# Kernel tuning notes

Hardware: AMD Instinct MI355X
Metric: run time of the kernel (lower is better)

The kernel has to match this reference:

```python
import jax, jax.numpy as jnp
import numpy as np

H, DH, M = 8, 64, 3          # heads, dim_head, num memory tokens
DIM = 512                    # model dim
INNER = H * DH               # 512
SCALE = DH ** -0.5
SQRT_DH = float(np.sqrt(DH))
SQRT_M = float(np.sqrt(M))


def setup_inputs() -> dict:
    key = jax.random.key(0)
    ks = jax.random.split(key, 7)
    b, n = 2, 2048
    x = jax.random.normal(ks[0], (b, n, DIM), dtype=jnp.float32)
    # Linear weights stored as (in, out); y = x @ W
    wq = jax.random.normal(ks[1], (DIM, INNER), dtype=jnp.float32) * (DIM ** -0.5)
    wkv = jax.random.normal(ks[2], (DIM, 2 * INNER), dtype=jnp.float32) * (DIM ** -0.5)
    wo = jax.random.normal(ks[3], (INNER, DIM), dtype=jnp.float32) * (INNER ** -0.5)
    bo = jnp.zeros((DIM,), dtype=jnp.float32)
    # xavier_normal_ std = sqrt(2 / (fan_in + fan_out)) over last two dims (M, INNER)
    xav = float(np.sqrt(2.0 / (M + INNER)))
    m_k = jax.random.normal(ks[4], (1, M, INNER), dtype=jnp.float32) * xav
    m_v = jax.random.normal(ks[5], (1, M, INNER), dtype=jnp.float32) * xav
    return {"x": x, "wq": wq, "wkv": wkv, "wo": wo, "bo": bo, "m_k": m_k, "m_v": m_v}


def reference(x, wq, wkv, wo, bo, m_k, m_v):
    b, n, _ = x.shape
    # projections -> (b, h, n, d)
    q = (x @ wq).reshape(b, n, H, DH).transpose(0, 2, 1, 3)
    kv = x @ wkv
    k, v = jnp.split(kv, 2, axis=-1)
    k = k.reshape(b, n, H, DH).transpose(0, 2, 1, 3)
    v = v.reshape(b, n, H, DH).transpose(0, 2, 1, 3)
    # memory tokens: torch does expand(b, M, INNER).view(b, H, M, DH),
    # a flat reshape (NOT a per-head rearrange) -- replicate exactly.
    mk = SQRT_DH * jnp.broadcast_to(m_k, (b, M, INNER)).reshape(b, H, M, DH)
    mv = SQRT_M * jnp.broadcast_to(m_v, (b, M, INNER)).reshape(b, H, M, DH)
    k = jnp.concatenate([k, mk], axis=2)  # (b, h, n+M, d)
    v = jnp.concatenate([v, mv], axis=2)
    dots = jnp.einsum('bhid,bhjd->bhij', q, k) * SCALE  # (b, h, n, n+M)
    attn = jax.nn.softmax(dots, axis=-1)                # dropout = identity (eval)
    out = jnp.einsum('bhij,bhjd->bhid', attn, v)
    out = out.transpose(0, 2, 1, 3).reshape(b, n, INNER)
    return out @ wo + bo
```

## Files before the change

kernel.cpp:

```cpp
#include <hip/hip_runtime.h>

typedef unsigned short u16;
typedef unsigned int u32;
typedef __attribute__((ext_vector_type(8))) __bf16 bf16x8;
typedef __attribute__((ext_vector_type(4))) float f32x4;

#define DEVI __device__ __forceinline__
#define C1 0.180336880f
#define C2 (-23.0831200f)

DEVI float bf2f(u16 u) {
    unsigned int v = ((unsigned int)u) << 16;
    return __uint_as_float(v);
}
DEVI u16 f2bf(float f) {
    unsigned int x = __float_as_uint(f);
    x += 0x7fffu + ((x >> 16) & 1u);
    return (u16)(x >> 16);
}
DEVI u32 pk2(float lo, float hi) {
    union { __bf16 b[2]; u32 u; } c;
    c.b[0] = (__bf16)lo; c.b[1] = (__bf16)hi;
    return c.u;
}
DEVI bf16x8 ldb8(const u16* p) {
    union { uint4 u; bf16x8 b; } c;
    c.u = *(const uint4*)p;
    return c.b;
}
DEVI f32x4 mfma32(bf16x8 a, bf16x8 b, f32x4 c) {
    return __builtin_amdgcn_mfma_f32_16x16x32_bf16(a, b, c, 0, 0, 0);
}
DEVI float clamp4(float v) { return fminf(fmaxf(v, -1e4f), 1e4f); }
DEVI float fexp2(float x) { return __builtin_amdgcn_exp2f(x); }
DEVI void gld16(const u16* g, u16* l) {
    __builtin_amdgcn_global_load_lds(
        (const __attribute__((address_space(1))) void*)g,
        (__attribute__((address_space(3))) void*)l, 16, 0, 0);
}

__global__ __launch_bounds__(256) void prep(
    const float* __restrict__ wq, const float* __restrict__ wkv,
    const float* __restrict__ wo, const float* __restrict__ x,
    const float* __restrict__ mkf, const float* __restrict__ mvf,
    u16* __restrict__ wqkvT, u16* __restrict__ woT, u16* __restrict__ xb,
    u16* __restrict__ qkv)
{
    const int bid = blockIdx.x, tid = threadIdx.x;
    if (bid < 256) {
        __shared__ u16 T[64][68];
        int j0, k0; const float* W; int ldw; u16* Out;
        if (bid < 192) { int jt = bid % 24, kt = bid / 24;
            j0 = jt * 64; k0 = kt * 64;
            if (j0 < 512) { W = wq + j0;          ldw = 512;  }
            else          { W = wkv + (j0 - 512); ldw = 1024; }
            Out = wqkvT;
        } else { int t = bid - 192;
            j0 = (t >> 3) * 64; k0 = (t & 7) * 64;
            W = wo + j0; ldw = 512; Out = woT;
        }
        const int lr = tid >> 4, lc = tid & 15;
        #pragma unroll
        for (int i = 0; i < 4; ++i) {
            int k = lr + i * 16;
            float4 v = *(const float4*)(W + (size_t)(k0 + k) * ldw + lc * 4);
            u16 p[4] = { f2bf(v.x), f2bf(v.y), f2bf(v.z), f2bf(v.w) };
            *(uint2*)&T[k][lc * 4] = *(uint2*)p;
        }
        __syncthreads();
        #pragma unroll
        for (int i = 0; i < 4; ++i) {
            int j = lr + i * 16;
            u16 p[4];
            #pragma unroll
            for (int c = 0; c < 4; ++c) p[c] = T[lc * 4 + c][j];
            *(uint2*)(Out + (size_t)(j0 + j) * 512 + k0 + lc * 4) = *(uint2*)p;
        }
    } else if (bid < 2304) {
        int e = (bid - 256) * 1024 + tid * 4;
        float4 v = *(const float4*)(x + e);
        u16 p[4] = { f2bf(v.x), f2bf(v.y), f2bf(v.z), f2bf(v.w) };
        *(uint2*)(xb + e) = *(uint2*)p;
    } else {
        int e = (bid - 2304) * 256 + tid;
        int b = e >> 16, rem = e & 65535;
        int row2 = rem >> 10, c = rem & 1023;
        float v = 0.f;
        if (row2 < 3) {
            int hh = (c & 511) >> 6, d = c & 63;
            int src = hh * 192 + row2 * 64 + d;
            v = (c < 512) ? 8.0f * mkf[src] : 1.7320508f * mvf[src];
        }
        qkv[((size_t)b * 2112 + 2048 + row2) * 1536 + 512 + c] = f2bf(v);
    }
}

template<int WNT, bool F32OUT>
__global__ __launch_bounds__(256) void gemm128(
    const u16* __restrict__ A, int lda,
    const u16* __restrict__ BT, int ldb,
    void* __restrict__ Cv, int ldc,
    const float* __restrict__ bias, int K, int mpad)
{
    constexpr int TN = 32 * WNT;
    __shared__ u16 As[128 * 32];
    __shared__ u16 Bs[TN * 32];

    const int tid = threadIdx.x;
    const int m0 = blockIdx.x * 128, n0 = blockIdx.y * TN;
    const int w = tid >> 6, lane = tid & 63, l15 = lane & 15, quad = lane >> 4;
    const int wr = w >> 1, wc = w & 1;

    const int srow = w * 16 + (lane >> 2), scg = (lane & 3) * 8;

    f32x4 acc[4][WNT];
    #pragma unroll
    for (int i = 0; i < 4; ++i)
        #pragma unroll
        for (int j = 0; j < WNT; ++j) acc[i][j] = (f32x4){0.f, 0.f, 0.f, 0.f};

    const u16* aG0 = A + (size_t)(m0 + srow) * lda + scg;
    const u16* aG1 = A + (size_t)(m0 + 64 + srow) * lda + scg;
    const u16* bG0 = BT + (size_t)(n0 + srow) * ldb + scg;
    const u16* bG1 = (WNT == 4) ? BT + (size_t)(n0 + 64 + srow) * ldb + scg : bG0;

    for (int k0 = 0; k0 < K; k0 += 32) {
        __syncthreads();
        gld16(aG0, &As[w * 512]);
        gld16(aG1, &As[2048 + w * 512]);
        gld16(bG0, &Bs[w * 512]);
        if (WNT == 4) gld16(bG1, &Bs[2048 + w * 512]);
        aG0 += 32; aG1 += 32; bG0 += 32; bG1 += 32;
        __syncthreads();

        bf16x8 af[4], bf[WNT];
        #pragma unroll
        for (int i = 0; i < 4; ++i)
            af[i] = ldb8(&As[(wr * 64 + 16 * i + l15) * 32 + quad * 8]);
        #pragma unroll
        for (int j = 0; j < WNT; ++j)
            bf[j] = ldb8(&Bs[(wc * (TN / 2) + 16 * j + l15) * 32 + quad * 8]);
        #pragma unroll
        for (int i = 0; i < 4; ++i)
            #pragma unroll
            for (int j = 0; j < WNT; ++j)
                acc[i][j] = mfma32(af[i], bf[j], acc[i][j]);
    }

    #pragma unroll
    for (int j = 0; j < WNT; ++j) {
        int col = n0 + wc * (TN / 2) + 16 * j + l15;
        float bv = bias ? bias[col] : 0.f;
        #pragma unroll
        for (int i = 0; i < 4; ++i) {
            #pragma unroll
            for (int r = 0; r < 4; ++r) {
                int row = m0 + wr * 64 + 16 * i + quad * 4 + r;
                int orow = row + ((row >> 11) * mpad);
                float vr = clamp4(acc[i][j][r] + bv);
                if (F32OUT) ((float*)Cv)[(size_t)orow * ldc + col] = vr;
                else        ((u16*)Cv)[(size_t)orow * ldc + col] = f2bf(vr);
            }
        }
    }
}

__global__ __launch_bounds__(256, 5) void attn_kernel(
    const u16* __restrict__ qkv, u16* __restrict__ Opart,
    float* __restrict__ Lpart)
{
    __shared__ alignas(16) u16 Ks[64][72];
    __shared__ alignas(16) u16 Vt[80][72];
    __shared__ alignas(16) u16 Ps[64][72];

    const int tid = threadIdx.x;
    const int bx = blockIdx.x;
    const int qt = bx / 5, s = bx - qt * 5;
    const int h = blockIdx.y, b = blockIdx.z;
    const int w = tid >> 6, lane = tid & 63, l15 = lane & 15, quad = lane >> 4;
    const size_t bq = (size_t)b * 2112;
    const int rq = qt * 64;
    const int ro = b * 2048 + qt * 64;

    {
        int row = 64 + (tid >> 4), col = (tid & 15) * 4;
        uint2 ones = { 0x3F803F80u, 0x3F803F80u };
        *(uint2*)&Vt[row][col] = ones;
    }
    {
        int row = tid >> 2, cg = (tid & 3) * 16;
        const u16* src = qkv + (bq + rq + row) * 1536 + h * 64 + cg;
        *(uint4*)&Ks[row][cg]     = *(const uint4*)src;
        *(uint4*)&Ks[row][cg + 8] = *(const uint4*)(src + 8);
    }
    __syncthreads();
    bf16x8 qf[2];
    qf[0] = ldb8(&Ks[16 * w + l15][quad * 8]);
    qf[1] = ldb8(&Ks[16 * w + l15][32 + quad * 8]);

    f32x4 O[4], O5;
    for (int t = 0; t < 4; ++t) O[t] = (f32x4){0.f, 0.f, 0.f, 0.f};
    O5 = (f32x4){0.f, 0.f, 0.f, 0.f};

    const int krow = tid >> 2, kcg = (tid & 3) * 16;
    const int vkp = (tid & 31) * 2, vdg = ((tid >> 5) & 7) * 8;

    const int kt0 = 7 * s - (s > 3 ? s - 3 : 0);
    const int kt1 = kt0 + (s < 3 ? 7 : 6);
    for (int kt = kt0; kt < kt1; ++kt) {
        __syncthreads();
        const u16* ksrc = qkv + (bq + kt * 64 + krow) * 1536 + 512 + h * 64 + kcg;
        uint4 k0 = *(const uint4*)ksrc, k1 = *(const uint4*)(ksrc + 8);
        const u16* vsrc = qkv + (bq + kt * 64 + vkp) * 1536 + 1024 + h * 64 + vdg;
        uint4 v0 = *(const uint4*)vsrc, v1 = *(const uint4*)(vsrc + 1536);
        *(uint4*)&Ks[krow][kcg]     = k0;
        *(uint4*)&Ks[krow][kcg + 8] = k1;
        {
            u32 a0[4] = {v0.x, v0.y, v0.z, v0.w};
            u32 a1[4] = {v1.x, v1.y, v1.z, v1.w};
            #pragma unroll
            for (int i = 0; i < 4; ++i) {
                u32 lo = __builtin_amdgcn_perm(a1[i], a0[i], 0x05040100u);
                u32 hi = __builtin_amdgcn_perm(a1[i], a0[i], 0x07060302u);
                *(u32*)&Vt[vdg + 2 * i][vkp]     = lo;
                *(u32*)&Vt[vdg + 2 * i + 1][vkp] = hi;
            }
        }
        __syncthreads();

        f32x4 d4[4];
        for (int t = 0; t < 4; ++t) d4[t] = (f32x4){0.f, 0.f, 0.f, 0.f};
        #pragma unroll
        for (int ks = 0; ks < 2; ++ks) {
            #pragma unroll
            for (int t = 0; t < 4; ++t) {
                bf16x8 kf = ldb8(&Ks[16 * t + l15][ks * 32 + quad * 8]);
                d4[t] = mfma32(kf, qf[ks], d4[t]);
            }
        }
        if (kt == 32) {
            #pragma unroll
            for (int t = 1; t < 4; ++t)
                d4[t] = (f32x4){-1e9f, -1e9f, -1e9f, -1e9f};
            #pragma unroll
            for (int r = 0; r < 4; ++r)
                if (!(quad == 0 && r < 3)) d4[0][r] = -1e9f;
        }

        #pragma unroll
        for (int t = 0; t < 4; ++t) {
            float p0 = fexp2(fmaf(d4[t][0], C1, C2));
            float p1 = fexp2(fmaf(d4[t][1], C1, C2));
            float p2 = fexp2(fmaf(d4[t][2], C1, C2));
            float p3 = fexp2(fmaf(d4[t][3], C1, C2));
            uint2 pv = { pk2(p0, p1), pk2(p2, p3) };
            *(uint2*)&Ps[16 * w + l15][16 * t + 4 * quad] = pv;
        }
        #pragma unroll
        for (int ks = 0; ks < 2; ++ks) {
            bf16x8 af = ldb8(&Ps[16 * w + l15][ks * 32 + quad * 8]);
            #pragma unroll
            for (int dt = 0; dt < 4; ++dt) {
                bf16x8 vf = ldb8(&Vt[16 * dt + l15][ks * 32 + quad * 8]);
                O[dt] = mfma32(af, vf, O[dt]);
            }
            bf16x8 of = ldb8(&Vt[64 + l15][ks * 32 + quad * 8]);
            O5 = mfma32(af, of, O5);
        }
    }

    u16* Ob = Opart + (size_t)s * 4096 * 512;
    #pragma unroll
    for (int r = 0; r < 4; ++r) {
        int row = ro + 16 * w + quad * 4 + r;
        #pragma unroll
        for (int dt = 0; dt < 4; ++dt)
            Ob[(size_t)row * 512 + h * 64 + 16 * dt + l15] = f2bf(O[dt][r]);
        if (l15 == 0)
            Lpart[((size_t)s * 4096 + row) * 8 + h] = O5[r];
    }
}

__global__ __launch_bounds__(256) void merge_kernel(
    const u16* __restrict__ Opart, const float* __restrict__ Lpart,
    u16* __restrict__ outp)
{
    int e = (blockIdx.x * 256 + threadIdx.x) * 4;
    int row = e >> 9, h = (e & 511) >> 6;
    float ax = 0.f, ay = 0.f, az = 0.f, aw = 0.f, l = 0.f;
    #pragma unroll
    for (int s = 0; s < 5; ++s) {
        uint2 pv = *(const uint2*)(Opart + (size_t)s * 4096 * 512 + e);
        ax += bf2f((u16)(pv.x & 0xffff)); ay += bf2f((u16)(pv.x >> 16));
        az += bf2f((u16)(pv.y & 0xffff)); aw += bf2f((u16)(pv.y >> 16));
        l += Lpart[((size_t)s * 4096 + row) * 8 + h];
    }
    float rl = 1.0f / fmaxf(l, 1e-30f);
    u16 p[4] = { f2bf(clamp4(ax * rl)), f2bf(clamp4(ay * rl)),
                 f2bf(clamp4(az * rl)), f2bf(clamp4(aw * rl)) };
    *(uint2*)(outp + e) = *(uint2*)p;
}

extern "C" void kernel_launch(void* const* d_in, const int* in_sizes, int n_in,
                              void* d_out, int out_size, void* d_ws, size_t ws_size,
                              hipStream_t stream)
{
    (void)in_sizes; (void)n_in; (void)out_size; (void)ws_size;
    const float* x   = (const float*)d_in[0];
    const float* wq  = (const float*)d_in[1];
    const float* wkv = (const float*)d_in[2];
    const float* wo  = (const float*)d_in[3];
    const float* bo  = (const float*)d_in[4];
    const float* mk  = (const float*)d_in[5];
    const float* mv  = (const float*)d_in[6];
    float* out = (float*)d_out;

    u16* qkv   = (u16*)d_ws;
    u16* outp  = qkv + 6488064;
    u16* woT   = outp + 2097152;
    float* Lpart = (float*)(woT + 262144);
    u16* scratch = (u16*)(Lpart + 163840);
    u16* wqkvT = scratch;
    u16* xb    = scratch + 786432;
    u16* Opart = scratch;

    prep<<<2816, 256, 0, stream>>>(wq, wkv, wo, x, mk, mv, wqkvT, woT, xb, qkv);
    gemm128<4, false><<<dim3(32, 12), 256, 0, stream>>>(
        xb, 512, wqkvT, 512, qkv, 1536, nullptr, 512, 64);
    attn_kernel<<<dim3(160, 8, 2), 256, 0, stream>>>(qkv, Opart, Lpart);
    merge_kernel<<<2048, 256, 0, stream>>>(Opart, Lpart, outp);
    gemm128<2, true><<<dim3(32, 8), 256, 0, stream>>>(
        outp, 512, woT, 512, out, 512, bo, 512, 0);
}
```

Before: 145.1 us.

## Process 128 query rows per attention block to reuse K/V tiles, split KV four ways

Each attention block now handles two 64-row query subtiles (A and B) against each loaded K/V tile, halving global K/V loads per query row. The KV split drops from 5 to 4 ranges (8-9 tiles each), the grid shrinks from 160 to 64 blocks along x, and the merge loops over 4 partials. Global loads for the next tile are issued before the first barrier so their latency can overlap the barrier wait. The cost is doubled accumulator registers with occupancy lowered to 4 waves per SIMD, and fewer blocks overall (1024 vs 2560).

New measurement: 138.0 us. -4.9%, faster.

```diff
diff --git a/kernel.cpp b/kernel.cpp
--- a/kernel.cpp
+++ b/kernel.cpp
@@ -165,22 +165,22 @@
     }
 }
 
-__global__ __launch_bounds__(256, 5) void attn_kernel(
+__global__ __launch_bounds__(256, 4) void attn_kernel(
     const u16* __restrict__ qkv, u16* __restrict__ Opart,
     float* __restrict__ Lpart)
 {
     __shared__ alignas(16) u16 Ks[64][72];
     __shared__ alignas(16) u16 Vt[80][72];
-    __shared__ alignas(16) u16 Ps[64][72];
+    __shared__ alignas(16) u16 Ps[128][72];
 
     const int tid = threadIdx.x;
     const int bx = blockIdx.x;
-    const int qt = bx / 5, s = bx - qt * 5;
+    const int qt = bx >> 2, s = bx & 3;
     const int h = blockIdx.y, b = blockIdx.z;
     const int w = tid >> 6, lane = tid & 63, l15 = lane & 15, quad = lane >> 4;
     const size_t bq = (size_t)b * 2112;
-    const int rq = qt * 64;
-    const int ro = b * 2048 + qt * 64;
+    const int rq = qt * 128;
+    const int ro = b * 2048 + qt * 128;
 
     {
         int row = 64 + (tid >> 4), col = (tid & 15) * 4;
@@ -188,31 +188,40 @@
         *(uint2*)&Vt[row][col] = ones;
     }
     {
-        int row = tid >> 2, cg = (tid & 3) * 16;
+        int row = tid >> 1, cg = (tid & 1) * 32;
         const u16* src = qkv + (bq + rq + row) * 1536 + h * 64 + cg;
-        *(uint4*)&Ks[row][cg]     = *(const uint4*)src;
-        *(uint4*)&Ks[row][cg + 8] = *(const uint4*)(src + 8);
+        *(uint4*)&Ps[row][cg]      = *(const uint4*)src;
+        *(uint4*)&Ps[row][cg + 8]  = *(const uint4*)(src + 8);
+        *(uint4*)&Ps[row][cg + 16] = *(const uint4*)(src + 16);
+        *(uint4*)&Ps[row][cg + 24] = *(const uint4*)(src + 24);
     }
     __syncthreads();
-    bf16x8 qf[2];
-    qf[0] = ldb8(&Ks[16 * w + l15][quad * 8]);
-    qf[1] = ldb8(&Ks[16 * w + l15][32 + quad * 8]);
-
-    f32x4 O[4], O5;
-    for (int t = 0; t < 4; ++t) O[t] = (f32x4){0.f, 0.f, 0.f, 0.f};
-    O5 = (f32x4){0.f, 0.f, 0.f, 0.f};
+    bf16x8 qfA[2], qfB[2];
+    qfA[0] = ldb8(&Ps[16 * w + l15][quad * 8]);
+    qfA[1] = ldb8(&Ps[16 * w + l15][32 + quad * 8]);
+    qfB[0] = ldb8(&Ps[64 + 16 * w + l15][quad * 8]);
+    qfB[1] = ldb8(&Ps[64 + 16 * w + l15][32 + quad * 8]);
+
+    f32x4 OA[4], OB[4], O5A, O5B;
+    #pragma unroll
+    for (int t = 0; t < 4; ++t) {
+        OA[t] = (f32x4){0.f, 0.f, 0.f, 0.f};
+        OB[t] = (f32x4){0.f, 0.f, 0.f, 0.f};
+    }
+    O5A = (f32x4){0.f, 0.f, 0.f, 0.f};
+    O5B = (f32x4){0.f, 0.f, 0.f, 0.f};
 
     const int krow = tid >> 2, kcg = (tid & 3) * 16;
     const int vkp = (tid & 31) * 2, vdg = ((tid >> 5) & 7) * 8;
 
-    const int kt0 = 7 * s - (s > 3 ? s - 3 : 0);
-    const int kt1 = kt0 + (s < 3 ? 7 : 6);
+    const int kt0 = s ? 8 * s + 1 : 0;
+    const int kt1 = 8 * s + 9;
     for (int kt = kt0; kt < kt1; ++kt) {
-        __syncthreads();
         const u16* ksrc = qkv + (bq + kt * 64 + krow) * 1536 + 512 + h * 64 + kcg;
         uint4 k0 = *(const uint4*)ksrc, k1 = *(const uint4*)(ksrc + 8);
         const u16* vsrc = qkv + (bq + kt * 64 + vkp) * 1536 + 1024 + h * 64 + vdg;
         uint4 v0 = *(const uint4*)vsrc, v1 = *(const uint4*)(vsrc + 1536);
+        __syncthreads();
         *(uint4*)&Ks[krow][kcg]     = k0;
         *(uint4*)&Ks[krow][kcg + 8] = k1;
         {
@@ -228,56 +237,76 @@
         }
         __syncthreads();
 
-        f32x4 d4[4];
-        for (int t = 0; t < 4; ++t) d4[t] = (f32x4){0.f, 0.f, 0.f, 0.f};
+        f32x4 dA[4], dB[4];
+        #pragma unroll
+        for (int t = 0; t < 4; ++t) {
+            dA[t] = (f32x4){0.f, 0.f, 0.f, 0.f};
+            dB[t] = (f32x4){0.f, 0.f, 0.f, 0.f};
+        }
         #pragma unroll
         for (int ks = 0; ks < 2; ++ks) {
             #pragma unroll
             for (int t = 0; t < 4; ++t) {
                 bf16x8 kf = ldb8(&Ks[16 * t + l15][ks * 32 + quad * 8]);
-                d4[t] = mfma32(kf, qf[ks], d4[t]);
+                dA[t] = mfma32(kf, qfA[ks], dA[t]);
+                dB[t] = mfma32(kf, qfB[ks], dB[t]);
             }
         }
         if (kt == 32) {
             #pragma unroll
-            for (int t = 1; t < 4; ++t)
-                d4[t] = (f32x4){-1e9f, -1e9f, -1e9f, -1e9f};
+            for (int t = 1; t < 4; ++t) {
+                dA[t] = (f32x4){-1e9f, -1e9f, -1e9f, -1e9f};
+                dB[t] = (f32x4){-1e9f, -1e9f, -1e9f, -1e9f};
+            }
             #pragma unroll
             for (int r = 0; r < 4; ++r)
-                if (!(quad == 0 && r < 3)) d4[0][r] = -1e9f;
+                if (!(quad == 0 && r < 3)) { dA[0][r] = -1e9f; dB[0][r] = -1e9f; }
         }
 
         #pragma unroll
         for (int t = 0; t < 4; ++t) {
-            float p0 = fexp2(fmaf(d4[t][0], C1, C2));
-            float p1 = fexp2(fmaf(d4[t][1], C1, C2));
-            float p2 = fexp2(fmaf(d4[t][2], C1, C2));
-            float p3 = fexp2(fmaf(d4[t][3], C1, C2));
-            uint2 pv = { pk2(p0, p1), pk2(p2, p3) };
-            *(uint2*)&Ps[16 * w + l15][16 * t + 4 * quad] = pv;
+            uint2 pa = { pk2(fexp2(fmaf(dA[t][0], C1, C2)),
+                             fexp2(fmaf(dA[t][1], C1, C2))),
+                         pk2(fexp2(fmaf(dA[t][2], C1, C2)),
+                             fexp2(fmaf(dA[t][3], C1, C2))) };
+            *(uint2*)&Ps[16 * w + l15][16 * t + 4 * quad] = pa;
+            uint2 pb = { pk2(fexp2(fmaf(dB[t][0], C1, C2)),
+                             fexp2(fmaf(dB[t][1], C1, C2))),
+                         pk2(fexp2(fmaf(dB[t][2], C1, C2)),
+                             fexp2(fmaf(dB[t][3], C1, C2))) };
+            *(uint2*)&Ps[64 + 16 * w + l15][16 * t + 4 * quad] = pb;
         }
         #pragma unroll
         for (int ks = 0; ks < 2; ++ks) {
-            bf16x8 af = ldb8(&Ps[16 * w + l15][ks * 32 + quad * 8]);
+            bf16x8 afA = ldb8(&Ps[16 * w + l15][ks * 32 + quad * 8]);
+            bf16x8 afB = ldb8(&Ps[64 + 16 * w + l15][ks * 32 + quad * 8]);
             #pragma unroll
             for (int dt = 0; dt < 4; ++dt) {
                 bf16x8 vf = ldb8(&Vt[16 * dt + l15][ks * 32 + quad * 8]);
-                O[dt] = mfma32(af, vf, O[dt]);
+                OA[dt] = mfma32(afA, vf, OA[dt]);
+                OB[dt] = mfma32(afB, vf, OB[dt]);
             }
             bf16x8 of = ldb8(&Vt[64 + l15][ks * 32 + quad * 8]);
-            O5 = mfma32(af, of, O5);
+            O5A = mfma32(afA, of, O5A);
+            O5B = mfma32(afB, of, O5B);
         }
     }
 
     u16* Ob = Opart + (size_t)s * 4096 * 512;
     #pragma unroll
     for (int r = 0; r < 4; ++r) {
-        int row = ro + 16 * w + quad * 4 + r;
-        #pragma unroll
-        for (int dt = 0; dt < 4; ++dt)
-            Ob[(size_t)row * 512 + h * 64 + 16 * dt + l15] = f2bf(O[dt][r]);
-        if (l15 == 0)
-            Lpart[((size_t)s * 4096 + row) * 8 + h] = O5[r];
+        int rowA = ro + 16 * w + quad * 4 + r;
+        int rowB = rowA + 64;
+        #pragma unroll
+        for (int dt = 0; dt < 4; ++dt) {
+            int col = h * 64 + 16 * dt + l15;
+            Ob[(size_t)rowA * 512 + col] = f2bf(OA[dt][r]);
+            Ob[(size_t)rowB * 512 + col] = f2bf(OB[dt][r]);
+        }
+        if (l15 == 0) {
+            Lpart[((size_t)s * 4096 + rowA) * 8 + h] = O5A[r];
+            Lpart[((size_t)s * 4096 + rowB) * 8 + h] = O5B[r];
+        }
     }
 }
 
@@ -289,7 +318,7 @@
     int row = e >> 9, h = (e & 511) >> 6;
     float ax = 0.f, ay = 0.f, az = 0.f, aw = 0.f, l = 0.f;
     #pragma unroll
-    for (int s = 0; s < 5; ++s) {
+    for (int s = 0; s < 4; ++s) {
         uint2 pv = *(const uint2*)(Opart + (size_t)s * 4096 * 512 + e);
         ax += bf2f((u16)(pv.x & 0xffff)); ay += bf2f((u16)(pv.x >> 16));
         az += bf2f((u16)(pv.y & 0xffff)); aw += bf2f((u16)(pv.y >> 16));
@@ -327,7 +356,7 @@
     prep<<<2816, 256, 0, stream>>>(wq, wkv, wo, x, mk, mv, wqkvT, woT, xb, qkv);
     gemm128<4, false><<<dim3(32, 12), 256, 0, stream>>>(
         xb, 512, wqkvT, 512, qkv, 1536, nullptr, 512, 64);
-    attn_kernel<<<dim3(160, 8, 2), 256, 0, stream>>>(qkv, Opart, Lpart);
+    attn_kernel<<<dim3(64, 8, 2), 256, 0, stream>>>(qkv, Opart, Lpart);
     merge_kernel<<<2048, 256, 0, stream>>>(Opart, Lpart, outp);
     gemm128<2, true><<<dim3(32, 8), 256, 0, stream>>>(
         outp, 512, woT, 512, out, 512, bo, 512, 0);
```

## Enlarge attention query tile to 256 rows and deepen GEMM K-step

Applied to the files above, without the earlier changes.

Each attention block now processes 256 query rows (four 64-row sub-tiles) against each K/V tile, so every loaded K/V tile is reused four times. The KV split drops from 5 to 4 parts, and merge is adjusted to match. The GEMMs are generalised to a TM×TN template with a 64-wide K step split across two LDS buffers, which halves the barriers per K, and they use smaller N tiles so more blocks launch. The price is more registers in attention (occupancy hint lowered from 5 to 2), more LDS for Ps, and fewer attention blocks (512 vs 2560).

After: 135.8 us. 1.07x faster.

```diff
diff --git a/kernel.cpp b/kernel.cpp
--- a/kernel.cpp
+++ b/kernel.cpp
@@ -95,67 +95,75 @@
     }
 }
 
-template<int WNT, bool F32OUT>
-__global__ __launch_bounds__(256) void gemm128(
+template<int TM, int TN, bool F32OUT>
+__global__ __launch_bounds__(256) void gemmK(
     const u16* __restrict__ A, int lda,
     const u16* __restrict__ BT, int ldb,
     void* __restrict__ Cv, int ldc,
     const float* __restrict__ bias, int K, int mpad)
 {
-    constexpr int TN = 32 * WNT;
-    __shared__ u16 As[128 * 32];
-    __shared__ u16 Bs[TN * 32];
+    constexpr int IL = TM / 32, JL = TN / 32;
+    __shared__ u16 As0[TM * 32], As1[TM * 32];
+    __shared__ u16 Bs0[TN * 32], Bs1[TN * 32];
 
     const int tid = threadIdx.x;
-    const int m0 = blockIdx.x * 128, n0 = blockIdx.y * TN;
+    const int m0 = blockIdx.x * TM, n0 = blockIdx.y * TN;
     const int w = tid >> 6, lane = tid & 63, l15 = lane & 15, quad = lane >> 4;
     const int wr = w >> 1, wc = w & 1;
-
-    const int srow = w * 16 + (lane >> 2), scg = (lane & 3) * 8;
-
-    f32x4 acc[4][WNT];
-    #pragma unroll
-    for (int i = 0; i < 4; ++i)
-        #pragma unroll
-        for (int j = 0; j < WNT; ++j) acc[i][j] = (f32x4){0.f, 0.f, 0.f, 0.f};
-
-    const u16* aG0 = A + (size_t)(m0 + srow) * lda + scg;
-    const u16* aG1 = A + (size_t)(m0 + 64 + srow) * lda + scg;
-    const u16* bG0 = BT + (size_t)(n0 + srow) * ldb + scg;
-    const u16* bG1 = (WNT == 4) ? BT + (size_t)(n0 + 64 + srow) * ldb + scg : bG0;
-
-    for (int k0 = 0; k0 < K; k0 += 32) {
-        __syncthreads();
-        gld16(aG0, &As[w * 512]);
-        gld16(aG1, &As[2048 + w * 512]);
-        gld16(bG0, &Bs[w * 512]);
-        if (WNT == 4) gld16(bG1, &Bs[2048 + w * 512]);
-        aG0 += 32; aG1 += 32; bG0 += 32; bG1 += 32;
-        __syncthreads();
-
-        bf16x8 af[4], bf[WNT];
-        #pragma unroll
-        for (int i = 0; i < 4; ++i)
-            af[i] = ldb8(&As[(wr * 64 + 16 * i + l15) * 32 + quad * 8]);
-        #pragma unroll
-        for (int j = 0; j < WNT; ++j)
-            bf[j] = ldb8(&Bs[(wc * (TN / 2) + 16 * j + l15) * 32 + quad * 8]);
-        #pragma unroll
-        for (int i = 0; i < 4; ++i)
-            #pragma unroll
-            for (int j = 0; j < WNT; ++j)
-                acc[i][j] = mfma32(af[i], bf[j], acc[i][j]);
-    }
-
-    #pragma unroll
-    for (int j = 0; j < WNT; ++j) {
+    const int sr = lane >> 2, sc = (lane & 3) * 8;
+
+    f32x4 acc[IL][JL];
+    #pragma unroll
+    for (int i = 0; i < IL; ++i)
+        #pragma unroll
+        for (int j = 0; j < JL; ++j) acc[i][j] = (f32x4){0.f, 0.f, 0.f, 0.f};
+
+    for (int k0 = 0; k0 < K; k0 += 64) {
+        __syncthreads();
+        #pragma unroll
+        for (int p = 0; p < TM / 64; ++p) {
+            int r0 = w * (TM / 4) + p * 16;
+            const u16* g = A + (size_t)(m0 + r0 + sr) * lda + k0 + sc;
+            gld16(g,      &As0[r0 * 32]);
+            gld16(g + 32, &As1[r0 * 32]);
+        }
+        #pragma unroll
+        for (int p = 0; p < TN / 64; ++p) {
+            int r0 = w * (TN / 4) + p * 16;
+            const u16* g = BT + (size_t)(n0 + r0 + sr) * ldb + k0 + sc;
+            gld16(g,      &Bs0[r0 * 32]);
+            gld16(g + 32, &Bs1[r0 * 32]);
+        }
+        __syncthreads();
+
+        #pragma unroll
+        for (int ks = 0; ks < 2; ++ks) {
+            const u16* Asel = ks ? As1 : As0;
+            const u16* Bsel = ks ? Bs1 : Bs0;
+            bf16x8 af[IL], bf[JL];
+            #pragma unroll
+            for (int i = 0; i < IL; ++i)
+                af[i] = ldb8(&Asel[(wr * (TM / 2) + 16 * i + l15) * 32 + quad * 8]);
+            #pragma unroll
+            for (int j = 0; j < JL; ++j)
+                bf[j] = ldb8(&Bsel[(wc * (TN / 2) + 16 * j + l15) * 32 + quad * 8]);
+            #pragma unroll
+            for (int i = 0; i < IL; ++i)
+                #pragma unroll
+                for (int j = 0; j < JL; ++j)
+                    acc[i][j] = mfma32(af[i], bf[j], acc[i][j]);
+        }
+    }
+
+    #pragma unroll
+    for (int j = 0; j < JL; ++j) {
         int col = n0 + wc * (TN / 2) + 16 * j + l15;
         float bv = bias ? bias[col] : 0.f;
         #pragma unroll
-        for (int i = 0; i < 4; ++i) {
+        for (int i = 0; i < IL; ++i) {
             #pragma unroll
             for (int r = 0; r < 4; ++r) {
-                int row = m0 + wr * 64 + 16 * i + quad * 4 + r;
+                int row = m0 + wr * (TM / 2) + 16 * i + quad * 4 + r;
                 int orow = row + ((row >> 11) * mpad);
                 float vr = clamp4(acc[i][j][r] + bv);
                 if (F32OUT) ((float*)Cv)[(size_t)orow * ldc + col] = vr;
@@ -165,22 +173,22 @@
     }
 }
 
-__global__ __launch_bounds__(256, 5) void attn_kernel(
+__global__ __launch_bounds__(256, 2) void attn_kernel(
     const u16* __restrict__ qkv, u16* __restrict__ Opart,
     float* __restrict__ Lpart)
 {
     __shared__ alignas(16) u16 Ks[64][72];
     __shared__ alignas(16) u16 Vt[80][72];
-    __shared__ alignas(16) u16 Ps[64][72];
+    __shared__ alignas(16) u16 Ps[256][72];
 
     const int tid = threadIdx.x;
     const int bx = blockIdx.x;
-    const int qt = bx / 5, s = bx - qt * 5;
+    const int qt = bx >> 2, s = bx & 3;
     const int h = blockIdx.y, b = blockIdx.z;
     const int w = tid >> 6, lane = tid & 63, l15 = lane & 15, quad = lane >> 4;
     const size_t bq = (size_t)b * 2112;
-    const int rq = qt * 64;
-    const int ro = b * 2048 + qt * 64;
+    const int rq = qt * 256;
+    const int ro = b * 2048 + qt * 256;
 
     {
         int row = 64 + (tid >> 4), col = (tid & 15) * 4;
@@ -188,31 +196,38 @@
         *(uint2*)&Vt[row][col] = ones;
     }
     {
-        int row = tid >> 2, cg = (tid & 3) * 16;
-        const u16* src = qkv + (bq + rq + row) * 1536 + h * 64 + cg;
-        *(uint4*)&Ks[row][cg]     = *(const uint4*)src;
-        *(uint4*)&Ks[row][cg + 8] = *(const uint4*)(src + 8);
+        const u16* src = qkv + (bq + rq + tid) * 1536 + h * 64;
+        #pragma unroll
+        for (int i = 0; i < 8; ++i)
+            *(uint4*)&Ps[tid][8 * i] = *(const uint4*)(src + 8 * i);
     }
     __syncthreads();
-    bf16x8 qf[2];
-    qf[0] = ldb8(&Ks[16 * w + l15][quad * 8]);
-    qf[1] = ldb8(&Ks[16 * w + l15][32 + quad * 8]);
-
-    f32x4 O[4], O5;
-    for (int t = 0; t < 4; ++t) O[t] = (f32x4){0.f, 0.f, 0.f, 0.f};
-    O5 = (f32x4){0.f, 0.f, 0.f, 0.f};
+    bf16x8 qf[4][2];
+    #pragma unroll
+    for (int sub = 0; sub < 4; ++sub) {
+        qf[sub][0] = ldb8(&Ps[64 * sub + 16 * w + l15][quad * 8]);
+        qf[sub][1] = ldb8(&Ps[64 * sub + 16 * w + l15][32 + quad * 8]);
+    }
+
+    f32x4 Od[4][4], Ol[4];
+    #pragma unroll
+    for (int sub = 0; sub < 4; ++sub) {
+        #pragma unroll
+        for (int t = 0; t < 4; ++t) Od[sub][t] = (f32x4){0.f, 0.f, 0.f, 0.f};
+        Ol[sub] = (f32x4){0.f, 0.f, 0.f, 0.f};
+    }
 
     const int krow = tid >> 2, kcg = (tid & 3) * 16;
     const int vkp = (tid & 31) * 2, vdg = ((tid >> 5) & 7) * 8;
 
-    const int kt0 = 7 * s - (s > 3 ? s - 3 : 0);
-    const int kt1 = kt0 + (s < 3 ? 7 : 6);
+    const int kt0 = s ? 8 * s + 1 : 0;
+    const int kt1 = 8 * s + 9;
     for (int kt = kt0; kt < kt1; ++kt) {
-        __syncthreads();
         const u16* ksrc = qkv + (bq + kt * 64 + krow) * 1536 + 512 + h * 64 + kcg;
         uint4 k0 = *(const uint4*)ksrc, k1 = *(const uint4*)(ksrc + 8);
         const u16* vsrc = qkv + (bq + kt * 64 + vkp) * 1536 + 1024 + h * 64 + vdg;
         uint4 v0 = *(const uint4*)vsrc, v1 = *(const uint4*)(vsrc + 1536);
+        __syncthreads();
         *(uint4*)&Ks[krow][kcg]     = k0;
         *(uint4*)&Ks[krow][kcg + 8] = k1;
         {
@@ -228,56 +243,77 @@
         }
         __syncthreads();
 
-        f32x4 d4[4];
-        for (int t = 0; t < 4; ++t) d4[t] = (f32x4){0.f, 0.f, 0.f, 0.f};
+        f32x4 d[4][4];
+        #pragma unroll
+        for (int sub = 0; sub < 4; ++sub)
+            #pragma unroll
+            for (int t = 0; t < 4; ++t) d[sub][t] = (f32x4){0.f, 0.f, 0.f, 0.f};
         #pragma unroll
         for (int ks = 0; ks < 2; ++ks) {
             #pragma unroll
             for (int t = 0; t < 4; ++t) {
                 bf16x8 kf = ldb8(&Ks[16 * t + l15][ks * 32 + quad * 8]);
-                d4[t] = mfma32(kf, qf[ks], d4[t]);
+                #pragma unroll
+                for (int sub = 0; sub < 4; ++sub)
+                    d[sub][t] = mfma32(kf, qf[sub][ks], d[sub][t]);
             }
         }
         if (kt == 32) {
             #pragma unroll
-            for (int t = 1; t < 4; ++t)
-                d4[t] = (f32x4){-1e9f, -1e9f, -1e9f, -1e9f};
-            #pragma unroll
-            for (int r = 0; r < 4; ++r)
-                if (!(quad == 0 && r < 3)) d4[0][r] = -1e9f;
-        }
-
-        #pragma unroll
-        for (int t = 0; t < 4; ++t) {
-            float p0 = fexp2(fmaf(d4[t][0], C1, C2));
-            float p1 = fexp2(fmaf(d4[t][1], C1, C2));
-            float p2 = fexp2(fmaf(d4[t][2], C1, C2));
-            float p3 = fexp2(fmaf(d4[t][3], C1, C2));
-            uint2 pv = { pk2(p0, p1), pk2(p2, p3) };
-            *(uint2*)&Ps[16 * w + l15][16 * t + 4 * quad] = pv;
-        }
+            for (int sub = 0; sub < 4; ++sub) {
+                #pragma unroll
+                for (int t = 1; t < 4; ++t)
+                    d[sub][t] = (f32x4){-1e9f, -1e9f, -1e9f, -1e9f};
+                #pragma unroll
+                for (int r = 0; r < 4; ++r)
+                    if (!(quad == 0 && r < 3)) d[sub][0][r] = -1e9f;
+            }
+        }
+
+        #pragma unroll
+        for (int sub = 0; sub < 4; ++sub)
+            #pragma unroll
+            for (int t = 0; t < 4; ++t) {
+                uint2 pv = { pk2(fexp2(fmaf(d[sub][t][0], C1, C2)),
+                                 fexp2(fmaf(d[sub][t][1], C1, C2))),
+                             pk2(fexp2(fmaf(d[sub][t][2], C1, C2)),
+                                 fexp2(fmaf(d[sub][t][3], C1, C2))) };
+                *(uint2*)&Ps[64 * sub + 16 * w + l15][16 * t + 4 * quad] = pv;
+            }
         #pragma unroll
         for (int ks = 0; ks < 2; ++ks) {
-            bf16x8 af = ldb8(&Ps[16 * w + l15][ks * 32 + quad * 8]);
+            bf16x8 af[4];
+            #pragma unroll
+            for (int sub = 0; sub < 4; ++sub)
+                af[sub] = ldb8(&Ps[64 * sub + 16 * w + l15][ks * 32 + quad * 8]);
             #pragma unroll
             for (int dt = 0; dt < 4; ++dt) {
                 bf16x8 vf = ldb8(&Vt[16 * dt + l15][ks * 32 + quad * 8]);
-                O[dt] = mfma32(af, vf, O[dt]);
+                #pragma unroll
+                for (int sub = 0; sub < 4; ++sub)
+                    Od[sub][dt] = mfma32(af[sub], vf, Od[sub][dt]);
             }
             bf16x8 of = ldb8(&Vt[64 + l15][ks * 32 + quad * 8]);
-            O5 = mfma32(af, of, O5);
+            #pragma unroll
+            for (int sub = 0; sub < 4; ++sub)
+                Ol[sub] = mfma32(af[sub], of, Ol[sub]);
         }
     }
 
     u16* Ob = Opart + (size_t)s * 4096 * 512;
     #pragma unroll
-    for (int r = 0; r < 4; ++r) {
-        int row = ro + 16 * w + quad * 4 + r;
-        #pragma unroll
-        for (int dt = 0; dt < 4; ++dt)
-            Ob[(size_t)row * 512 + h * 64 + 16 * dt + l15] = f2bf(O[dt][r]);
-        if (l15 == 0)
-            Lpart[((size_t)s * 4096 + row) * 8 + h] = O5[r];
+    for (int sub = 0; sub < 4; ++sub) {
+        #pragma unroll
+        for (int r = 0; r < 4; ++r) {
+            int row = ro + 64 * sub + 16 * w + quad * 4 + r;
+            #pragma unroll
+            for (int dt = 0; dt < 4; ++dt) {
+                int col = h * 64 + 16 * dt + l15;
+                Ob[(size_t)row * 512 + col] = f2bf(Od[sub][dt][r]);
+            }
+            if (l15 == 0)
+                Lpart[((size_t)s * 4096 + row) * 8 + h] = Ol[sub][r];
+        }
     }
 }
 
@@ -289,7 +325,7 @@
     int row = e >> 9, h = (e & 511) >> 6;
     float ax = 0.f, ay = 0.f, az = 0.f, aw = 0.f, l = 0.f;
     #pragma unroll
-    for (int s = 0; s < 5; ++s) {
+    for (int s = 0; s < 4; ++s) {
         uint2 pv = *(const uint2*)(Opart + (size_t)s * 4096 * 512 + e);
         ax += bf2f((u16)(pv.x & 0xffff)); ay += bf2f((u16)(pv.x >> 16));
         az += bf2f((u16)(pv.y & 0xffff)); aw += bf2f((u16)(pv.y >> 16));
@@ -325,10 +361,10 @@
     u16* Opart = scratch;
 
     prep<<<2816, 256, 0, stream>>>(wq, wkv, wo, x, mk, mv, wqkvT, woT, xb, qkv);
-    gemm128<4, false><<<dim3(32, 12), 256, 0, stream>>>(
+    gemmK<128, 64, false><<<dim3(32, 24), 256, 0, stream>>>(
         xb, 512, wqkvT, 512, qkv, 1536, nullptr, 512, 64);
-    attn_kernel<<<dim3(160, 8, 2), 256, 0, stream>>>(qkv, Opart, Lpart);
+    attn_kernel<<<dim3(32, 8, 2), 256, 0, stream>>>(qkv, Opart, Lpart);
     merge_kernel<<<2048, 256, 0, stream>>>(Opart, Lpart, outp);
-    gemm128<2, true><<<dim3(32, 8), 256, 0, stream>>>(
+    gemmK<64, 64, true><<<dim3(64, 8), 256, 0, stream>>>(
         outp, 512, woT, 512, out, 512, bo, 512, 0);
 }
```
